# Performance work log

Measured on AMD Instinct MI355X. Metric: run time of the kernel, lower is better.

## Reference

```python
import jax, jax.numpy as jnp
import numpy as np

B, S, D = 8, 2048, 512
FF = 2048
E = 8

def setup_inputs() -> dict:
    key = jax.random.key(0)
    ks = jax.random.split(key, 7)
    s = 1.0 / np.sqrt(D)
    sf = 1.0 / np.sqrt(FF)
    return {
        "x":  jax.random.normal(ks[0], (B, S, D), dtype=jnp.float32),
        "Wg": jax.random.uniform(ks[1], (D, E), jnp.float32, -s, s),
        "bg": jax.random.uniform(ks[2], (E,), jnp.float32, -s, s),
        "W1": jax.random.uniform(ks[3], (E, D, FF), jnp.float32, -s, s),
        "b1": jax.random.uniform(ks[4], (E, FF), jnp.float32, -s, s),
        "W2": jax.random.uniform(ks[5], (E, FF, D), jnp.float32, -sf, sf),
        "b2": jax.random.uniform(ks[6], (E, D), jnp.float32, -sf, sf),
    }

def reference(x, Wg, bg, W1, b1, W2, b2):
    b, s, d = x.shape
    xf = x.reshape(-1, d)                      # [T, D]
    logits = xf @ Wg + bg                      # [T, E]
    probs = jax.nn.softmax(logits, axis=-1)
    pmax = jnp.max(probs, axis=-1)             # [T]
    routes = jnp.argmax(probs, axis=-1)        # [T] int
    xs = xf * pmax[:, None]                    # scale tokens by router prob
    # per-expert FFN over all tokens, select the routed expert's output
    out_tok = jnp.zeros_like(xf)
    for e in range(E):
        h = jax.nn.relu(xs @ W1[e] + b1[e])    # [T, FF]
        y = h @ W2[e] + b2[e]                  # [T, D]
        out_tok = jnp.where((routes == e)[:, None], y, out_tok)
    # torch.cat of per-expert nonzero-index gathers == tokens stably sorted by expert id
    order = jnp.argsort(routes)                # jnp.argsort is stable
    return out_tok[order].reshape(b, s, d)
```

## Files before the change

### kernel.cpp

```cpp
#include <hip/hip_runtime.h>
#include <hip/hip_bf16.h>

constexpr int TTOK  = 16384;
constexpr int DDIM  = 512;
constexpr int FFDIM = 2048;
constexpr int NEXP  = 8;
constexpr int GB_TOK = 16;
constexpr int NGB    = TTOK / GB_TOK;
constexpr int MAXTILES = TTOK / 128 + NEXP;
constexpr int TRW1_BLOCKS = 4096;
constexpr int TRW2_XBLK   = 256;

typedef __attribute__((ext_vector_type(8))) short short8_t;
typedef __attribute__((ext_vector_type(4))) float f32x4_t;

__device__ __forceinline__ unsigned short f2bf(float f) {
    union { float f; unsigned u; } v; v.f = f;
    return (unsigned short)((v.u + 0x7fffu + ((v.u >> 16) & 1u)) >> 16);
}

__device__ __forceinline__ void gl_lds16(const void* g, void* l) {
    __builtin_amdgcn_global_load_lds(
        (const __attribute__((address_space(1))) void*)g,
        (__attribute__((address_space(3))) void*)l,
        16, 0, 0);
}

__device__ __forceinline__ void tr_tile(const float* __restrict__ src,
                                        unsigned short* __restrict__ dst,
                                        int R, int C, int tileId, float* lds) {
    int tilesC = C / 32;
    int c0 = (tileId % tilesC) * 32;
    int r0 = (tileId / tilesC) * 64;
    int t = threadIdx.x;
    int lr = t >> 3;
    int ls = t & 7;
    #pragma unroll
    for (int rb = 0; rb < 2; rb++) {
        int row = rb * 32 + lr;
        float4 v = *(const float4*)(src + (size_t)(r0 + row) * C + c0 + 4 * ls);
        int p4 = (4 * ls) ^ (8 * ((row >> 3) & 3));
        *(float4*)(lds + row * 36 + p4) = v;
    }
    __syncthreads();
    int c = t >> 3;
    int b = t & 7;
    union { short8_t v; unsigned short s[8]; } o;
    #pragma unroll
    for (int j = 0; j < 8; j++) {
        int r = 8 * b + j;
        int p = c ^ (8 * ((r >> 3) & 3));
        o.s[j] = f2bf(lds[r * 36 + p]);
    }
    *(short8_t*)(dst + (size_t)(c0 + c) * R + r0 + 8 * b) = o.v;
}

__global__ __launch_bounds__(256) void prep_kernel(const float* __restrict__ x,
                                                   const float* __restrict__ Wg,
                                                   const float* __restrict__ bg,
                                                   int* __restrict__ route,
                                                   float* __restrict__ pmax,
                                                   int* __restrict__ blockCounts,
                                                   const float* __restrict__ W1,
                                                   unsigned short* __restrict__ W1T) {
    int tid = threadIdx.x;
    if (blockIdx.x >= NGB) {
        __shared__ __align__(16) float tlds[64 * 36];
        int id = blockIdx.x - NGB;
        int e = id >> 9;
        int tile = id & 511;
        tr_tile(W1 + (size_t)e * DDIM * FFDIM, W1T + (size_t)e * DDIM * FFDIM,
                DDIM, FFDIM, tile, tlds);
        return;
    }
    __shared__ int cnt[NEXP];
    __shared__ float bgs[NEXP];
    int gb = blockIdx.x;
    if (tid < NEXP) { cnt[tid] = 0; bgs[tid] = bg[tid]; }
    __syncthreads();
    int wave = tid >> 6, lane = tid & 63;
    float w[8][8];
    #pragma unroll
    for (int jj = 0; jj < 8; jj++) {
        float4 a = *(const float4*)(Wg + (size_t)(lane * 8 + jj) * NEXP);
        float4 b = *(const float4*)(Wg + (size_t)(lane * 8 + jj) * NEXP + 4);
        w[jj][0] = a.x; w[jj][1] = a.y; w[jj][2] = a.z; w[jj][3] = a.w;
        w[jj][4] = b.x; w[jj][5] = b.y; w[jj][6] = b.z; w[jj][7] = b.w;
    }
    int tbase = gb * GB_TOK + wave * 4;
    for (int it = 0; it < 4; it++) {
        int t = tbase + it;
        float4 xa = *(const float4*)(x + (size_t)t * DDIM + lane * 8);
        float4 xb = *(const float4*)(x + (size_t)t * DDIM + lane * 8 + 4);
        float xs[8] = {xa.x, xa.y, xa.z, xa.w, xb.x, xb.y, xb.z, xb.w};
        double acc[NEXP];
        #pragma unroll
        for (int e = 0; e < NEXP; e++) acc[e] = 0.0;
        #pragma unroll
        for (int jj = 0; jj < 8; jj++) {
            double xv = (double)xs[jj];
            #pragma unroll
            for (int e = 0; e < NEXP; e++) acc[e] += xv * (double)w[jj][e];
        }
        #pragma unroll
        for (int off = 32; off > 0; off >>= 1) {
            #pragma unroll
            for (int e = 0; e < NEXP; e++) acc[e] += __shfl_down(acc[e], off);
        }
        if (lane == 0) {
            double l[NEXP];
            #pragma unroll
            for (int e = 0; e < NEXP; e++) l[e] = acc[e] + (double)bgs[e];
            int r = 0; double lm = l[0];
            #pragma unroll
            for (int e = 1; e < NEXP; e++) if (l[e] > lm) { lm = l[e]; r = e; }
            double s = 0.0;
            #pragma unroll
            for (int e = 0; e < NEXP; e++) s += exp(l[e] - lm);
            route[t] = r;
            pmax[t] = (float)(1.0 / s);
            atomicAdd(&cnt[r], 1);
        }
    }
    __syncthreads();
    if (tid < NEXP) blockCounts[gb * NEXP + tid] = cnt[tid];
}

__global__ __launch_bounds__(1024) void scan_kernel(const int* __restrict__ blockCounts,
                                                    int* __restrict__ blockOffsets,
                                                    int* __restrict__ segPrefix,
                                                    int* __restrict__ tilePrefix) {
    int b = threadIdx.x, lane = b & 63, wv = b >> 6;
    int c[NEXP], s[NEXP];
    #pragma unroll
    for (int e = 0; e < NEXP; e++) { c[e] = blockCounts[b * NEXP + e]; s[e] = c[e]; }
    #pragma unroll
    for (int off = 1; off < 64; off <<= 1) {
        #pragma unroll
        for (int e = 0; e < NEXP; e++) {
            int t = __shfl_up(s[e], off);
            if (lane >= off) s[e] += t;
        }
    }
    __shared__ int wtot[16][NEXP];
    __shared__ int wpre[16][NEXP];
    __shared__ int base[NEXP + 1];
    if (lane == 63) {
        #pragma unroll
        for (int e = 0; e < NEXP; e++) wtot[wv][e] = s[e];
    }
    __syncthreads();
    if (wv == 0) {
        int t[NEXP];
        #pragma unroll
        for (int e = 0; e < NEXP; e++) t[e] = (lane < 16) ? wtot[lane][e] : 0;
        #pragma unroll
        for (int off = 1; off < 16; off <<= 1) {
            #pragma unroll
            for (int e = 0; e < NEXP; e++) {
                int u = __shfl_up(t[e], off);
                if (lane >= off) t[e] += u;
            }
        }
        if (lane < 16) {
            #pragma unroll
            for (int e = 0; e < NEXP; e++) wpre[lane][e] = t[e] - wtot[lane][e];
        }
        if (lane == 15) {
            int ssum = 0;
            #pragma unroll
            for (int e = 0; e < NEXP; e++) { base[e] = ssum; segPrefix[e] = ssum; ssum += t[e]; }
            base[NEXP] = ssum; segPrefix[NEXP] = ssum;
            int tp = 0; tilePrefix[0] = 0;
            #pragma unroll
            for (int e = 0; e < NEXP; e++) { tp += (t[e] + 127) >> 7; tilePrefix[e + 1] = tp; }
        }
    }
    __syncthreads();
    #pragma unroll
    for (int e = 0; e < NEXP; e++)
        blockOffsets[b * NEXP + e] = base[e] + wpre[wv][e] + s[e] - c[e];
}

__global__ __launch_bounds__(256) void scatter_kernel(const float* __restrict__ x,
                                                      const int* __restrict__ route,
                                                      const float* __restrict__ pmax,
                                                      const int* __restrict__ blockOffsets,
                                                      unsigned short* __restrict__ Xs) {
    __shared__ int dstL[GB_TOK];
    __shared__ float pmL[GB_TOK];
    int tid = threadIdx.x;
    int bb = blockIdx.x;
    if (tid < GB_TOK) {
        int t = bb * GB_TOK + tid;
        int r = route[t];
        unsigned long long ltmask = (tid == 0) ? 0ull : ((~0ull) >> (64 - tid));
        int rank = 0;
        #pragma unroll
        for (int e = 0; e < NEXP; e++) {
            unsigned long long m = __ballot(r == e);
            if (r == e) rank = __popcll(m & ltmask);
        }
        dstL[tid] = blockOffsets[bb * NEXP + r] + rank;
        pmL[tid] = pmax[t];
    }
    __syncthreads();
    int wave = tid >> 6, lane = tid & 63;
    for (int rr = 0; rr < 4; rr++) {
        int rowl = wave * 4 + rr;
        int t = bb * GB_TOK + rowl;
        float pm = pmL[rowl];
        const float4* xr = (const float4*)(x + (size_t)t * DDIM) + lane * 2;
        float4 a = xr[0], b = xr[1];
        union { short8_t v; unsigned short s[8]; } o;
        o.s[0] = f2bf(a.x * pm); o.s[1] = f2bf(a.y * pm);
        o.s[2] = f2bf(a.z * pm); o.s[3] = f2bf(a.w * pm);
        o.s[4] = f2bf(b.x * pm); o.s[5] = f2bf(b.y * pm);
        o.s[6] = f2bf(b.z * pm); o.s[7] = f2bf(b.w * pm);
        *(short8_t*)(Xs + (size_t)dstL[rowl] * DDIM + lane * 8) = o.v;
    }
}

__global__ __launch_bounds__(256) void gemm1_fused(const unsigned short* __restrict__ A,
                                                   const unsigned short* __restrict__ Bt,
                                                   const float* __restrict__ bias,
                                                   unsigned short* __restrict__ C,
                                                   const int* __restrict__ segPrefix,
                                                   const int* __restrict__ tilePrefix,
                                                   const float* __restrict__ W2,
                                                   unsigned short* __restrict__ W2T) {
    constexpr int K = DDIM, N = FFDIM;
    __shared__ __align__(16) unsigned short SMEM[16384];

    if (blockIdx.x >= MAXTILES) {
        int id = (blockIdx.x - MAXTILES) * 16 + blockIdx.y;
        int e = id >> 9;
        int tile = id & 511;
        tr_tile(W2 + (size_t)e * DDIM * FFDIM, W2T + (size_t)e * DDIM * FFDIM,
                FFDIM, DDIM, tile, (float*)SMEM);
        return;
    }

    int bx = blockIdx.x;
    bx = (bx & 7) * (MAXTILES / 8) + (bx >> 3);
    int t = bx;
    if (t >= tilePrefix[NEXP]) return;
    int e = 0;
    #pragma unroll
    for (int i = 1; i <= NEXP; i++) e += (t >= tilePrefix[i]) ? 1 : 0;
    int seg1 = segPrefix[e + 1];
    int m0 = segPrefix[e] + (t - tilePrefix[e]) * 128;
    int n0 = blockIdx.y * 128;

    unsigned short* As = SMEM;
    unsigned short* Bs = SMEM + 8192;

    int tid = threadIdx.x, wave = tid >> 6, lane = tid & 63;
    const unsigned short* Bte = Bt + (size_t)e * N * K;

    int srow = lane >> 2;
    int sg   = (lane & 3) ^ ((lane >> 2) & 3) ^ ((lane >> 4) & 3);
    int scol = sg * 8;

    f32x4_t acc[4][4];
    #pragma unroll
    for (int i = 0; i < 4; i++)
        #pragma unroll
        for (int j = 0; j < 4; j++) acc[i][j] = (f32x4_t){0.f, 0.f, 0.f, 0.f};

    int wm = (wave & 1) * 64;
    int wn = (wave >> 1) * 64;
    int frow = lane & 15;
    int gr = lane >> 4;
    int fswz = (gr ^ (frow & 3) ^ ((frow >> 2) & 3)) * 8;

    int reg0 = wave * 2;
    int arow0 = m0 + reg0 * 16 + srow;
    arow0 = arow0 < TTOK ? arow0 : TTOK - 1;
    int arow1 = m0 + (reg0 + 1) * 16 + srow;
    arow1 = arow1 < TTOK ? arow1 : TTOK - 1;
    const unsigned short* aptr0 = A + (size_t)arow0 * K + scol;
    const unsigned short* aptr1 = A + (size_t)arow1 * K + scol;
    const unsigned short* bptr0 = Bte + (size_t)(n0 + reg0 * 16 + srow) * K + scol;
    const unsigned short* bptr1 = Bte + (size_t)(n0 + (reg0 + 1) * 16 + srow) * K + scol;

    #pragma unroll
    for (int kc = 0; kc < K; kc += 64) {
        #pragma unroll
        for (int p = 0; p < 2; p++) {
            gl_lds16(aptr0 + kc + p * 32, &As[p * 4096 + reg0 * 512]);
            gl_lds16(aptr1 + kc + p * 32, &As[p * 4096 + (reg0 + 1) * 512]);
            gl_lds16(bptr0 + kc + p * 32, &Bs[p * 4096 + reg0 * 512]);
            gl_lds16(bptr1 + kc + p * 32, &Bs[p * 4096 + (reg0 + 1) * 512]);
        }
        __syncthreads();
        #pragma unroll
        for (int p = 0; p < 2; p++) {
            short8_t af[4], bfr[4];
            #pragma unroll
            for (int i = 0; i < 4; i++)
                af[i] = *(const short8_t*)&As[p * 4096 + (wm + i * 16 + frow) * 32 + fswz];
            #pragma unroll
            for (int j = 0; j < 4; j++)
                bfr[j] = *(const short8_t*)&Bs[p * 4096 + (wn + j * 16 + frow) * 32 + fswz];
            #pragma unroll
            for (int i = 0; i < 4; i++)
                #pragma unroll
                for (int j = 0; j < 4; j++)
                    acc[i][j] = __builtin_amdgcn_mfma_f32_16x16x32_bf16(af[i], bfr[j], acc[i][j], 0, 0, 0);
        }
        __syncthreads();
    }

    int quad = lane >> 4;
    int colb = lane & 15;
    float bv[4];
    #pragma unroll
    for (int j = 0; j < 4; j++) bv[j] = bias[(size_t)e * N + n0 + wn + j * 16 + colb];

    unsigned short* cbuf = As;
    #pragma unroll
    for (int p = 0; p < 2; p++) {
        __syncthreads();
        if ((wave >> 1) == p) {
            #pragma unroll
            for (int i = 0; i < 4; i++)
                #pragma unroll
                for (int j = 0; j < 4; j++)
                    #pragma unroll
                    for (int r = 0; r < 4; r++) {
                        float v = acc[i][j][r] + bv[j];
                        v = fmaxf(v, 0.0f);
                        int wrow = wm + i * 16 + quad * 4 + r;
                        int cc = (j * 16 + colb) ^ (((wrow >> 3) & 1) * 16);
                        cbuf[wrow * 72 + cc] = f2bf(v);
                    }
        }
        __syncthreads();
        int row = tid >> 1, ch = (tid & 1) * 32;
        int grow = m0 + row;
        if (grow < seg1) {
            #pragma unroll
            for (int k = 0; k < 4; k++) {
                int vv = (ch + k * 8) ^ (((row >> 3) & 1) * 16);
                short8_t v = *(const short8_t*)&cbuf[row * 72 + vv];
                *(short8_t*)&C[(size_t)grow * N + n0 + p * 64 + ch + k * 8] = v;
            }
        }
    }
}

template <bool RELU, typename OutT, int K, int N>
__global__ __launch_bounds__(256) void gemm_seg(const unsigned short* __restrict__ A,
                                                const unsigned short* __restrict__ Bt,
                                                const float* __restrict__ bias,
                                                OutT* __restrict__ C,
                                                const int* __restrict__ segPrefix,
                                                const int* __restrict__ tilePrefix) {
    int bx = blockIdx.x;
    bx = (bx & 7) * (MAXTILES / 8) + (bx >> 3);
    int t = bx;
    if (t >= tilePrefix[NEXP]) return;
    int e = 0;
    #pragma unroll
    for (int i = 1; i <= NEXP; i++) e += (t >= tilePrefix[i]) ? 1 : 0;
    int seg1 = segPrefix[e + 1];
    int m0 = segPrefix[e] + (t - tilePrefix[e]) * 128;
    int n0 = blockIdx.y * 128;

    __shared__ unsigned short As[2 * 4096];
    __shared__ unsigned short Bs[2 * 4096];

    int tid = threadIdx.x, wave = tid >> 6, lane = tid & 63;
    const unsigned short* Bte = Bt + (size_t)e * N * K;

    int srow = lane >> 2;
    int sg   = (lane & 3) ^ ((lane >> 2) & 3) ^ ((lane >> 4) & 3);
    int scol = sg * 8;

    f32x4_t acc[4][4];
    #pragma unroll
    for (int i = 0; i < 4; i++)
        #pragma unroll
        for (int j = 0; j < 4; j++) acc[i][j] = (f32x4_t){0.f, 0.f, 0.f, 0.f};

    int wm = (wave & 1) * 64;
    int wn = (wave >> 1) * 64;
    int frow = lane & 15;
    int gr = lane >> 4;
    int fswz = (gr ^ (frow & 3) ^ ((frow >> 2) & 3)) * 8;

    int reg0 = wave * 2;
    int arow0 = m0 + reg0 * 16 + srow;
    arow0 = arow0 < TTOK ? arow0 : TTOK - 1;
    int arow1 = m0 + (reg0 + 1) * 16 + srow;
    arow1 = arow1 < TTOK ? arow1 : TTOK - 1;
    const unsigned short* aptr0 = A + (size_t)arow0 * K + scol;
    const unsigned short* aptr1 = A + (size_t)arow1 * K + scol;
    const unsigned short* bptr0 = Bte + (size_t)(n0 + reg0 * 16 + srow) * K + scol;
    const unsigned short* bptr1 = Bte + (size_t)(n0 + (reg0 + 1) * 16 + srow) * K + scol;

    #pragma unroll
    for (int kc = 0; kc < K; kc += 64) {
        #pragma unroll
        for (int p = 0; p < 2; p++) {
            gl_lds16(aptr0 + kc + p * 32, &As[p * 4096 + reg0 * 512]);
            gl_lds16(aptr1 + kc + p * 32, &As[p * 4096 + (reg0 + 1) * 512]);
            gl_lds16(bptr0 + kc + p * 32, &Bs[p * 4096 + reg0 * 512]);
            gl_lds16(bptr1 + kc + p * 32, &Bs[p * 4096 + (reg0 + 1) * 512]);
        }
        __syncthreads();
        #pragma unroll
        for (int p = 0; p < 2; p++) {
            short8_t af[4], bfr[4];
            #pragma unroll
            for (int i = 0; i < 4; i++)
                af[i] = *(const short8_t*)&As[p * 4096 + (wm + i * 16 + frow) * 32 + fswz];
            #pragma unroll
            for (int j = 0; j < 4; j++)
                bfr[j] = *(const short8_t*)&Bs[p * 4096 + (wn + j * 16 + frow) * 32 + fswz];
            #pragma unroll
            for (int i = 0; i < 4; i++)
                #pragma unroll
                for (int j = 0; j < 4; j++)
                    acc[i][j] = __builtin_amdgcn_mfma_f32_16x16x32_bf16(af[i], bfr[j], acc[i][j], 0, 0, 0);
        }
        __syncthreads();
    }

    int quad = lane >> 4;
    int colb = lane & 15;
    float bv[4];
    #pragma unroll
    for (int j = 0; j < 4; j++) bv[j] = bias[(size_t)e * N + n0 + wn + j * 16 + colb];

    #pragma unroll
    for (int i = 0; i < 4; i++) {
        #pragma unroll
        for (int j = 0; j < 4; j++) {
            int col = n0 + wn + j * 16 + colb;
            #pragma unroll
            for (int r = 0; r < 4; r++) {
                int row = m0 + wm + i * 16 + quad * 4 + r;
                if (row < seg1) {
                    float v = acc[i][j][r] + bv[j];
                    if (RELU) v = fmaxf(v, 0.0f);
                    C[(size_t)row * N + col] = v;
                }
            }
        }
    }
}

extern "C" void kernel_launch(void* const* d_in, const int* in_sizes, int n_in,
                              void* d_out, int out_size, void* d_ws, size_t ws_size,
                              hipStream_t stream) {
    const float* x  = (const float*)d_in[0];
    const float* Wg = (const float*)d_in[1];
    const float* bg = (const float*)d_in[2];
    const float* W1 = (const float*)d_in[3];
    const float* b1 = (const float*)d_in[4];
    const float* W2 = (const float*)d_in[5];
    const float* b2 = (const float*)d_in[6];
    float* out = (float*)d_out;

    char* ws = (char*)d_ws;
    size_t off = 0;
    auto alloc = [&](size_t bytes) -> char* {
        char* p = ws + off;
        off += (bytes + 255) & ~(size_t)255;
        return p;
    };
    unsigned short* W1T = (unsigned short*)alloc((size_t)NEXP * DDIM * FFDIM * 2);
    unsigned short* W2T = (unsigned short*)alloc((size_t)NEXP * DDIM * FFDIM * 2);
    unsigned short* Xs  = (unsigned short*)alloc((size_t)TTOK * DDIM * 2);
    unsigned short* H   = (unsigned short*)alloc((size_t)TTOK * FFDIM * 2);
    int*   route        = (int*)alloc((size_t)TTOK * 4);
    float* pmaxArr      = (float*)alloc((size_t)TTOK * 4);
    int*   blockCounts  = (int*)alloc((size_t)NGB * NEXP * 4);
    int*   blockOffsets = (int*)alloc((size_t)NGB * NEXP * 4);
    int*   segPrefix    = (int*)alloc((size_t)(NEXP + 1) * 4);
    int*   tilePrefix   = (int*)alloc((size_t)(NEXP + 1) * 4);

    prep_kernel<<<NGB + TRW1_BLOCKS, 256, 0, stream>>>(
        x, Wg, bg, route, pmaxArr, blockCounts, W1, W1T);
    scan_kernel<<<1, NGB, 0, stream>>>(blockCounts, blockOffsets, segPrefix, tilePrefix);
    scatter_kernel<<<NGB, 256, 0, stream>>>(x, route, pmaxArr, blockOffsets, Xs);
    gemm1_fused<<<dim3(MAXTILES + TRW2_XBLK, FFDIM / 128, 1), 256, 0, stream>>>(
        Xs, W1T, b1, H, segPrefix, tilePrefix, W2, W2T);
    gemm_seg<false, float, FFDIM, DDIM><<<dim3(MAXTILES, DDIM / 128, 1), 256, 0, stream>>>(
        H, W2T, b2, out, segPrefix, tilePrefix);
}
```

Measured before the change: 294.5 us.

## Fold scan into scatter, narrow gemm2 N-tile, use float softmax sum

Drops the single-block scan kernel. Each scatter block now reduces the whole blockCounts array itself to get its own per-expert offsets, and block 0 writes the segment and tile prefixes. The second GEMM's N-tile shrinks from 128 to 64, which doubles the grid to fill more CUs and halves the B-tile LDS and accumulator registers. The router softmax denominator switches from double exp to float __expf. This trades a kernel launch for redundant count reads in every block, gemm2 for more A reloads, and pmax for slightly lower precision.

```diff
diff --git a/kernel.cpp b/kernel.cpp
--- a/kernel.cpp
+++ b/kernel.cpp
@@ -114,83 +114,79 @@
             int r = 0; double lm = l[0];
             #pragma unroll
             for (int e = 1; e < NEXP; e++) if (l[e] > lm) { lm = l[e]; r = e; }
-            double s = 0.0;
-            #pragma unroll
-            for (int e = 0; e < NEXP; e++) s += exp(l[e] - lm);
+            float s = 0.0f;
+            #pragma unroll
+            for (int e = 0; e < NEXP; e++) s += __expf((float)(l[e] - lm));
             route[t] = r;
-            pmax[t] = (float)(1.0 / s);
+            pmax[t] = 1.0f / s;
             atomicAdd(&cnt[r], 1);
         }
     }
     __syncthreads();
     if (tid < NEXP) blockCounts[gb * NEXP + tid] = cnt[tid];
-}
-
-__global__ __launch_bounds__(1024) void scan_kernel(const int* __restrict__ blockCounts,
-                                                    int* __restrict__ blockOffsets,
-                                                    int* __restrict__ segPrefix,
-                                                    int* __restrict__ tilePrefix) {
-    int b = threadIdx.x, lane = b & 63, wv = b >> 6;
-    int c[NEXP], s[NEXP];
-    #pragma unroll
-    for (int e = 0; e < NEXP; e++) { c[e] = blockCounts[b * NEXP + e]; s[e] = c[e]; }
-    #pragma unroll
-    for (int off = 1; off < 64; off <<= 1) {
-        #pragma unroll
-        for (int e = 0; e < NEXP; e++) {
-            int t = __shfl_up(s[e], off);
-            if (lane >= off) s[e] += t;
-        }
-    }
-    __shared__ int wtot[16][NEXP];
-    __shared__ int wpre[16][NEXP];
-    __shared__ int base[NEXP + 1];
-    if (lane == 63) {
-        #pragma unroll
-        for (int e = 0; e < NEXP; e++) wtot[wv][e] = s[e];
-    }
-    __syncthreads();
-    if (wv == 0) {
-        int t[NEXP];
-        #pragma unroll
-        for (int e = 0; e < NEXP; e++) t[e] = (lane < 16) ? wtot[lane][e] : 0;
-        #pragma unroll
-        for (int off = 1; off < 16; off <<= 1) {
-            #pragma unroll
-            for (int e = 0; e < NEXP; e++) {
-                int u = __shfl_up(t[e], off);
-                if (lane >= off) t[e] += u;
-            }
-        }
-        if (lane < 16) {
-            #pragma unroll
-            for (int e = 0; e < NEXP; e++) wpre[lane][e] = t[e] - wtot[lane][e];
-        }
-        if (lane == 15) {
-            int ssum = 0;
-            #pragma unroll
-            for (int e = 0; e < NEXP; e++) { base[e] = ssum; segPrefix[e] = ssum; ssum += t[e]; }
-            base[NEXP] = ssum; segPrefix[NEXP] = ssum;
-            int tp = 0; tilePrefix[0] = 0;
-            #pragma unroll
-            for (int e = 0; e < NEXP; e++) { tp += (t[e] + 127) >> 7; tilePrefix[e + 1] = tp; }
-        }
-    }
-    __syncthreads();
-    #pragma unroll
-    for (int e = 0; e < NEXP; e++)
-        blockOffsets[b * NEXP + e] = base[e] + wpre[wv][e] + s[e] - c[e];
 }
 
 __global__ __launch_bounds__(256) void scatter_kernel(const float* __restrict__ x,
                                                       const int* __restrict__ route,
                                                       const float* __restrict__ pmax,
-                                                      const int* __restrict__ blockOffsets,
-                                                      unsigned short* __restrict__ Xs) {
+                                                      const int* __restrict__ blockCounts,
+                                                      unsigned short* __restrict__ Xs,
+                                                      int* __restrict__ segPrefix,
+                                                      int* __restrict__ tilePrefix) {
+    int tid = threadIdx.x;
+    int bb = blockIdx.x;
+    int wave = tid >> 6, lane = tid & 63;
+
+    int tot[NEXP], pre[NEXP];
+    #pragma unroll
+    for (int e = 0; e < NEXP; e++) { tot[e] = 0; pre[e] = 0; }
+    for (int b = tid; b < NGB; b += 256) {
+        #pragma unroll
+        for (int e = 0; e < NEXP; e++) {
+            int c = blockCounts[b * NEXP + e];
+            tot[e] += c;
+            if (b < bb) pre[e] += c;
+        }
+    }
+    #pragma unroll
+    for (int off = 32; off > 0; off >>= 1) {
+        #pragma unroll
+        for (int e = 0; e < NEXP; e++) {
+            tot[e] += __shfl_down(tot[e], off);
+            pre[e] += __shfl_down(pre[e], off);
+        }
+    }
+    __shared__ int stot[4][NEXP], spre[4][NEXP];
+    __shared__ int boff[NEXP];
+    if (lane == 0) {
+        #pragma unroll
+        for (int e = 0; e < NEXP; e++) { stot[wave][e] = tot[e]; spre[wave][e] = pre[e]; }
+    }
+    __syncthreads();
+    if (tid == 0) {
+        int T[NEXP], P[NEXP];
+        #pragma unroll
+        for (int e = 0; e < NEXP; e++) {
+            T[e] = stot[0][e] + stot[1][e] + stot[2][e] + stot[3][e];
+            P[e] = spre[0][e] + spre[1][e] + spre[2][e] + spre[3][e];
+        }
+        int s = 0;
+        #pragma unroll
+        for (int e = 0; e < NEXP; e++) { boff[e] = s + P[e]; s += T[e]; }
+        if (bb == 0) {
+            int ss = 0, tp = 0;
+            segPrefix[0] = 0; tilePrefix[0] = 0;
+            #pragma unroll
+            for (int e = 0; e < NEXP; e++) {
+                ss += T[e]; tp += (T[e] + 127) >> 7;
+                segPrefix[e + 1] = ss; tilePrefix[e + 1] = tp;
+            }
+        }
+    }
+    __syncthreads();
+
     __shared__ int dstL[GB_TOK];
     __shared__ float pmL[GB_TOK];
-    int tid = threadIdx.x;
-    int bb = blockIdx.x;
     if (tid < GB_TOK) {
         int t = bb * GB_TOK + tid;
         int r = route[t];
@@ -201,11 +197,10 @@
             unsigned long long m = __ballot(r == e);
             if (r == e) rank = __popcll(m & ltmask);
         }
-        dstL[tid] = blockOffsets[bb * NEXP + r] + rank;
+        dstL[tid] = boff[r] + rank;
         pmL[tid] = pmax[t];
     }
     __syncthreads();
-    int wave = tid >> 6, lane = tid & 63;
     for (int rr = 0; rr < 4; rr++) {
         int rowl = wave * 4 + rr;
         int t = bb * GB_TOK + rowl;
@@ -350,13 +345,13 @@
     }
 }
 
-template <bool RELU, typename OutT, int K, int N>
-__global__ __launch_bounds__(256) void gemm_seg(const unsigned short* __restrict__ A,
-                                                const unsigned short* __restrict__ Bt,
-                                                const float* __restrict__ bias,
-                                                OutT* __restrict__ C,
-                                                const int* __restrict__ segPrefix,
-                                                const int* __restrict__ tilePrefix) {
+__global__ __launch_bounds__(256) void gemm2_seg(const unsigned short* __restrict__ A,
+                                                 const unsigned short* __restrict__ Bt,
+                                                 const float* __restrict__ bias,
+                                                 float* __restrict__ C,
+                                                 const int* __restrict__ segPrefix,
+                                                 const int* __restrict__ tilePrefix) {
+    constexpr int K = FFDIM, N = DDIM;
     int bx = blockIdx.x;
     bx = (bx & 7) * (MAXTILES / 8) + (bx >> 3);
     int t = bx;
@@ -366,10 +361,10 @@
     for (int i = 1; i <= NEXP; i++) e += (t >= tilePrefix[i]) ? 1 : 0;
     int seg1 = segPrefix[e + 1];
     int m0 = segPrefix[e] + (t - tilePrefix[e]) * 128;
-    int n0 = blockIdx.y * 128;
+    int n0 = blockIdx.y * 64;
 
     __shared__ unsigned short As[2 * 4096];
-    __shared__ unsigned short Bs[2 * 4096];
+    __shared__ unsigned short Bs[2 * 2048];
 
     int tid = threadIdx.x, wave = tid >> 6, lane = tid & 63;
     const unsigned short* Bte = Bt + (size_t)e * N * K;
@@ -378,14 +373,14 @@
     int sg   = (lane & 3) ^ ((lane >> 2) & 3) ^ ((lane >> 4) & 3);
     int scol = sg * 8;
 
-    f32x4_t acc[4][4];
+    f32x4_t acc[4][2];
     #pragma unroll
     for (int i = 0; i < 4; i++)
         #pragma unroll
-        for (int j = 0; j < 4; j++) acc[i][j] = (f32x4_t){0.f, 0.f, 0.f, 0.f};
+        for (int j = 0; j < 2; j++) acc[i][j] = (f32x4_t){0.f, 0.f, 0.f, 0.f};
 
     int wm = (wave & 1) * 64;
-    int wn = (wave >> 1) * 64;
+    int wn = (wave >> 1) * 32;
     int frow = lane & 15;
     int gr = lane >> 4;
     int fswz = (gr ^ (frow & 3) ^ ((frow >> 2) & 3)) * 8;
@@ -397,8 +392,7 @@
     arow1 = arow1 < TTOK ? arow1 : TTOK - 1;
     const unsigned short* aptr0 = A + (size_t)arow0 * K + scol;
     const unsigned short* aptr1 = A + (size_t)arow1 * K + scol;
-    const unsigned short* bptr0 = Bte + (size_t)(n0 + reg0 * 16 + srow) * K + scol;
-    const unsigned short* bptr1 = Bte + (size_t)(n0 + (reg0 + 1) * 16 + srow) * K + scol;
+    const unsigned short* bptrw = Bte + (size_t)(n0 + wave * 16 + srow) * K + scol;
 
     #pragma unroll
     for (int kc = 0; kc < K; kc += 64) {
@@ -406,23 +400,22 @@
         for (int p = 0; p < 2; p++) {
             gl_lds16(aptr0 + kc + p * 32, &As[p * 4096 + reg0 * 512]);
             gl_lds16(aptr1 + kc + p * 32, &As[p * 4096 + (reg0 + 1) * 512]);
-            gl_lds16(bptr0 + kc + p * 32, &Bs[p * 4096 + reg0 * 512]);
-            gl_lds16(bptr1 + kc + p * 32, &Bs[p * 4096 + (reg0 + 1) * 512]);
+            gl_lds16(bptrw + kc + p * 32, &Bs[p * 2048 + wave * 512]);
         }
         __syncthreads();
         #pragma unroll
         for (int p = 0; p < 2; p++) {
-            short8_t af[4], bfr[4];
+            short8_t af[4], bfr[2];
             #pragma unroll
             for (int i = 0; i < 4; i++)
                 af[i] = *(const short8_t*)&As[p * 4096 + (wm + i * 16 + frow) * 32 + fswz];
             #pragma unroll
-            for (int j = 0; j < 4; j++)
-                bfr[j] = *(const short8_t*)&Bs[p * 4096 + (wn + j * 16 + frow) * 32 + fswz];
+            for (int j = 0; j < 2; j++)
+                bfr[j] = *(const short8_t*)&Bs[p * 2048 + (wn + j * 16 + frow) * 32 + fswz];
             #pragma unroll
             for (int i = 0; i < 4; i++)
                 #pragma unroll
-                for (int j = 0; j < 4; j++)
+                for (int j = 0; j < 2; j++)
                     acc[i][j] = __builtin_amdgcn_mfma_f32_16x16x32_bf16(af[i], bfr[j], acc[i][j], 0, 0, 0);
         }
         __syncthreads();
@@ -430,21 +423,20 @@
 
     int quad = lane >> 4;
     int colb = lane & 15;
-    float bv[4];
-    #pragma unroll
-    for (int j = 0; j < 4; j++) bv[j] = bias[(size_t)e * N + n0 + wn + j * 16 + colb];
+    float bv[2];
+    #pragma unroll
+    for (int j = 0; j < 2; j++) bv[j] = bias[(size_t)e * N + n0 + wn + j * 16 + colb];
 
     #pragma unroll
     for (int i = 0; i < 4; i++) {
         #pragma unroll
-        for (int j = 0; j < 4; j++) {
+        for (int j = 0; j < 2; j++) {
             int col = n0 + wn + j * 16 + colb;
             #pragma unroll
             for (int r = 0; r < 4; r++) {
                 int row = m0 + wm + i * 16 + quad * 4 + r;
                 if (row < seg1) {
                     float v = acc[i][j][r] + bv[j];
-                    if (RELU) v = fmaxf(v, 0.0f);
                     C[(size_t)row * N + col] = v;
                 }
             }
@@ -478,16 +470,15 @@
     int*   route        = (int*)alloc((size_t)TTOK * 4);
     float* pmaxArr      = (float*)alloc((size_t)TTOK * 4);
     int*   blockCounts  = (int*)alloc((size_t)NGB * NEXP * 4);
-    int*   blockOffsets = (int*)alloc((size_t)NGB * NEXP * 4);
     int*   segPrefix    = (int*)alloc((size_t)(NEXP + 1) * 4);
     int*   tilePrefix   = (int*)alloc((size_t)(NEXP + 1) * 4);
 
     prep_kernel<<<NGB + TRW1_BLOCKS, 256, 0, stream>>>(
         x, Wg, bg, route, pmaxArr, blockCounts, W1, W1T);
-    scan_kernel<<<1, NGB, 0, stream>>>(blockCounts, blockOffsets, segPrefix, tilePrefix);
-    scatter_kernel<<<NGB, 256, 0, stream>>>(x, route, pmaxArr, blockOffsets, Xs);
+    scatter_kernel<<<NGB, 256, 0, stream>>>(
+        x, route, pmaxArr, blockCounts, Xs, segPrefix, tilePrefix);
     gemm1_fused<<<dim3(MAXTILES + TRW2_XBLK, FFDIM / 128, 1), 256, 0, stream>>>(
         Xs, W1T, b1, H, segPrefix, tilePrefix, W2, W2T);
-    gemm_seg<false, float, FFDIM, DDIM><<<dim3(MAXTILES, DDIM / 128, 1), 256, 0, stream>>>(
+    gemm2_seg<<<dim3(MAXTILES, DDIM / 64, 1), 256, 0, stream>>>(
         H, W2T, b2, out, segPrefix, tilePrefix);
 }
```

Measured after the change: 303.8 us. +3.2%, slower.
